# Kernel optimization log

Measured on AMD Instinct MI355X. Metric: run time of the kernel, lower is better.

## Reference

```python
import jax, jax.numpy as jnp
import numpy as np

EPS = 1e-12  # F.normalize eps

def _l2norm(t):
    n = jnp.linalg.norm(t, axis=-1, keepdims=True)
    return t / jnp.maximum(n, EPS)

def setup_inputs() -> dict:
    key = jax.random.key(0)
    ks = jax.random.split(key, 6)
    B, S, H, M = 4, 4096, 1024, 256
    x = jax.random.normal(ks[0], (B, S, H), dtype=jnp.float32)
    W_query = jax.random.normal(ks[1], (M, H), dtype=jnp.float32) * 0.02
    W_key = jax.random.normal(ks[2], (M, H), dtype=jnp.float32) * 0.02
    W_value = jax.random.normal(ks[3], (M, H), dtype=jnp.float32) * 0.02
    W_out = jax.random.normal(ks[4], (H, M), dtype=jnp.float32) * 0.02
    M0 = jnp.zeros((M, M), dtype=jnp.float32)
    return {"x": x, "W_query": W_query, "W_key": W_key, "W_value": W_value,
            "W_out": W_out, "M0": M0, "chunk_size": 64}

def reference(x, W_query, W_key, W_value, W_out, M0, chunk_size):
    B, S, H = x.shape
    Mdim = W_query.shape[0]
    decay, max_m_norm = 0.99, 10.0
    q = jnp.einsum('bsh,mh->bsm', x, W_query)
    k = _l2norm(jnp.einsum('bsh,mh->bsm', x, W_key))
    v = _l2norm(jnp.einsum('bsh,mh->bsm', x, W_value))
    n_chunks = S // chunk_size
    c = chunk_size
    # (n_chunks, B, c, Mdim) so scan iterates over chunks
    qc = q.reshape(B, n_chunks, c, Mdim).transpose(1, 0, 2, 3)
    kc = k.reshape(B, n_chunks, c, Mdim).transpose(1, 0, 2, 3)
    vc = v.reshape(B, n_chunks, c, Mdim).transpose(1, 0, 2, 3)

    def step(Mst, qkv):
        qch, kch, vch = qkv
        # read with state at start of chunk: q @ M.T
        r = jnp.einsum('bcm,nm->bcn', qch, Mst)
        # uniform write, token-level aggregation
        outer = jnp.einsum('bci,bcj->ij', vch, kch) / (B * c)
        Mn = decay * Mst + outer
        nrm = jnp.linalg.norm(Mn)
        Mn = Mn * (max_m_norm / jnp.maximum(nrm, max_m_norm))
        return Mn, r

    _, r_all = jax.lax.scan(step, M0, (qc, kc, vc))  # (n_chunks, B, c, Mdim)
    retrieved = r_all.transpose(1, 0, 2, 3).reshape(B, S, Mdim)
    out = jnp.einsum('bsm,hm->bsh', retrieved, W_out)
    return out
```

## Files before the change

### kernel.cpp

```cpp
#include <hip/hip_runtime.h>
#include <hip/hip_bf16.h>


typedef __attribute__((ext_vector_type(4))) float  f4;
typedef __attribute__((ext_vector_type(8))) short  bf16x8;

constexpr int   Hdim  = 1024;
constexpr int   Md    = 256;
constexpr int   Ttok  = 16384;
constexpr float DECAY = 0.99f;
constexpr float MAXN  = 10.0f;

__device__ __forceinline__ unsigned short f2bf(float f) {
  union { float f; unsigned u; } v; v.f = f;
  unsigned r = v.u + 0x7FFFu + ((v.u >> 16) & 1u);
  return (unsigned short)(r >> 16);
}
__device__ __forceinline__ float bf2f(unsigned short h) {
  union { unsigned u; float f; } v; v.u = ((unsigned)h) << 16; return v.f;
}
__device__ __forceinline__ unsigned pk2bf(float a, float b) {
  __hip_bfloat162 h = __float22bfloat162_rn(make_float2(a, b));
  unsigned u; __builtin_memcpy(&u, &h, 4); return u;
}
__device__ __forceinline__ void gll16(const void* gptr, void* lptr) {
  __builtin_amdgcn_global_load_lds(
      (const __attribute__((address_space(1))) unsigned int*)gptr,
      (__attribute__((address_space(3))) unsigned int*)lptr, 16, 0, 0);
}

__global__ __launch_bounds__(256) void k0_wcvt(
    const float* __restrict__ Wq, const float* __restrict__ Wk,
    const float* __restrict__ Wv, const float* __restrict__ Wo,
    unsigned short* __restrict__ Wb, unsigned short* __restrict__ Wob)
{
  int gid = blockIdx.x * 256 + threadIdx.x;
  const float* src; unsigned short* dst; int off;
  if (gid < 32768)      { src = Wq; dst = Wb;          off = gid; }
  else if (gid < 65536) { src = Wk; dst = Wb + 262144; off = gid - 32768; }
  else if (gid < 98304) { src = Wv; dst = Wb + 524288; off = gid - 65536; }
  else                  { src = Wo; dst = Wob;         off = gid - 98304; }
  float4 a = ((const float4*)src)[off * 2];
  float4 b = ((const float4*)src)[off * 2 + 1];
  ((uint4*)dst)[off] = make_uint4(pk2bf(a.x, a.y), pk2bf(a.z, a.w),
                                  pk2bf(b.x, b.y), pk2bf(b.z, b.w));
}

__global__ __launch_bounds__(256) void k1_proj(
    const float* __restrict__ x, const unsigned short* __restrict__ Wb,
    unsigned short* __restrict__ qp, unsigned short* __restrict__ kb,
    unsigned short* __restrict__ vb)
{
  __shared__ float          As[128 * 64];
  __shared__ unsigned short Bs[128 * 64];
  const int tid = threadIdx.x;
  const int g = blockIdx.x;
  const int xcd = g & 7, wq_ = g >> 3;
  const int ntile = wq_ % 6;
  const int strip = xcd * 16 + wq_ / 6;
  const int row0 = strip * 128;
  const int n0 = ntile * 128;
  const int seg = n0 >> 8;
  const int nw0 = n0 & 255;
  unsigned short* dst = (seg == 0) ? qp : ((seg == 1) ? kb : vb);

  const int lane = tid & 63, wid = tid >> 6;
  const int wm = wid & 1, wn = wid >> 1;
  const int lr = lane & 15, lq = lane >> 4;
  const int arow_l = lane >> 4, aseg_l = lane & 15;
  const int brow_l = lane >> 3, bseg_l = lane & 7;

  f4 acc[4][4];
#pragma unroll
  for (int i = 0; i < 4; ++i)
#pragma unroll
    for (int j = 0; j < 4; ++j) acc[i][j] = f4{0.f, 0.f, 0.f, 0.f};

  for (int kk = 0; kk < Hdim; kk += 64) {
#pragma unroll
    for (int i = 0; i < 8; ++i) {
      int r = wid * 32 + i * 4 + arow_l;
      int s = aseg_l ^ (r & 15);
      gll16(&x[(long)(row0 + r) * Hdim + kk + s * 4], &As[(wid * 32 + i * 4) * 64]);
    }
#pragma unroll
    for (int i = 0; i < 4; ++i) {
      int r = wid * 32 + i * 8 + brow_l;
      int s = bseg_l ^ (r & 7);
      gll16(&Wb[(long)(n0 + r) * Hdim + kk + s * 8], &Bs[(wid * 32 + i * 8) * 64]);
    }
    __syncthreads();
#pragma unroll
    for (int ks = 0; ks < 2; ++ks) {
      bf16x8 af[4], bfr[4];
#pragma unroll
      for (int i = 0; i < 4; ++i) {
        int m = wm * 64 + i * 16 + lr;
        int p0 = (ks * 8 + lq * 2) ^ (m & 15);
        int p1 = p0 ^ 1;
        f4 a0 = *(const f4*)&As[m * 64 + p0 * 4];
        f4 a1 = *(const f4*)&As[m * 64 + p1 * 4];
        union { bf16x8 v; unsigned u[4]; } au;
        au.u[0] = pk2bf(a0[0], a0[1]); au.u[1] = pk2bf(a0[2], a0[3]);
        au.u[2] = pk2bf(a1[0], a1[1]); au.u[3] = pk2bf(a1[2], a1[3]);
        af[i] = au.v;
      }
#pragma unroll
      for (int j = 0; j < 4; ++j) {
        int n = wn * 64 + j * 16 + lr;
        int pb = (ks * 4 + lq) ^ (n & 7);
        bfr[j] = *(const bf16x8*)&Bs[n * 64 + pb * 8];
      }
#pragma unroll
      for (int i = 0; i < 4; ++i)
#pragma unroll
        for (int j = 0; j < 4; ++j)
          acc[i][j] = __builtin_amdgcn_mfma_f32_16x16x32_bf16(af[i], bfr[j], acc[i][j], 0, 0, 0);
    }
    __syncthreads();
  }
#pragma unroll
  for (int i = 0; i < 4; ++i)
#pragma unroll
    for (int rr = 0; rr < 4; ++rr) {
      int token = row0 + wm * 64 + i * 16 + lq * 4 + rr;
      int b = token >> 12, s = token & 4095;
      int pidx = (s >> 6) * 256 + b * 64 + (s & 63);
#pragma unroll
      for (int j = 0; j < 4; ++j) {
        int nn = nw0 + wn * 64 + j * 16 + lr;
        dst[(long)pidx * Md + nn] = f2bf(acc[i][j][rr]);
      }
    }
}

__global__ __launch_bounds__(256) void k2_norms(
    const unsigned short* __restrict__ kb, const unsigned short* __restrict__ vb,
    float* __restrict__ innk, float* __restrict__ innv, float* __restrict__ D)
{
  const int tid = threadIdx.x;
  if (blockIdx.x == 0)
    for (int i = tid; i < 4096; i += 256) D[i] = 0.f;
  const int wid = tid >> 6, lane = tid & 63;
  const int row = blockIdx.x * 4 + wid;
  const unsigned short* p = (row < Ttok) ? (kb + (long)row * Md) : (vb + (long)(row - Ttok) * Md);
  ushort4 v = *(const ushort4*)&p[lane * 4];
  float f0 = bf2f(v.x), f1 = bf2f(v.y), f2 = bf2f(v.z), f3 = bf2f(v.w);
  float s = f0 * f0 + f1 * f1 + f2 * f2 + f3 * f3;
#pragma unroll
  for (int off = 32; off; off >>= 1) s += __shfl_xor(s, off);
  if (lane == 0) {
    float inv = 1.0f / fmaxf(sqrtf(s), 1e-12f);
    if (row < Ttok) innk[row] = inv; else innv[row - Ttok] = inv;
  }
}

__global__ __launch_bounds__(256) void k3_outer(
    const unsigned short* __restrict__ kb, const unsigned short* __restrict__ vb,
    const float* __restrict__ innk, const float* __restrict__ innv,
    float* __restrict__ O)
{
  __shared__ unsigned short Als[64][40];
  __shared__ unsigned short Bls[256][40];
  const int tid = threadIdx.x;
  const int t  = blockIdx.y;
  const int i0 = blockIdx.x * 64;
  const int lane = tid & 63, wid = tid >> 6;
  const int lr = lane & 15, lq = lane >> 4;

  f4 acc[16];
#pragma unroll
  for (int q = 0; q < 16; ++q) acc[q] = f4{0.f, 0.f, 0.f, 0.f};

  for (int tok0 = 0; tok0 < 256; tok0 += 32) {
    {
      int i4 = (tid & 15) * 4, tl0 = tid >> 4;
#pragma unroll
      for (int p = 0; p < 2; ++p) {
        int tl = tl0 + 16 * p;
        int pidx = t * 256 + tok0 + tl;
        float sc = innv[pidx];
        ushort4 vv = *(const ushort4*)&vb[(long)pidx * Md + i0 + i4];
        Als[i4 + 0][tl] = f2bf(bf2f(vv.x) * sc);
        Als[i4 + 1][tl] = f2bf(bf2f(vv.y) * sc);
        Als[i4 + 2][tl] = f2bf(bf2f(vv.z) * sc);
        Als[i4 + 3][tl] = f2bf(bf2f(vv.w) * sc);
      }
    }
    {
      int j4 = (tid & 63) * 4, tl0 = tid >> 6;
#pragma unroll
      for (int p = 0; p < 8; ++p) {
        int tl = tl0 + 4 * p;
        int pidx = t * 256 + tok0 + tl;
        float sc = innk[pidx];
        ushort4 kv = *(const ushort4*)&kb[(long)pidx * Md + j4];
        Bls[j4 + 0][tl] = f2bf(bf2f(kv.x) * sc);
        Bls[j4 + 1][tl] = f2bf(bf2f(kv.y) * sc);
        Bls[j4 + 2][tl] = f2bf(bf2f(kv.z) * sc);
        Bls[j4 + 3][tl] = f2bf(bf2f(kv.w) * sc);
      }
    }
    __syncthreads();
    bf16x8 af = *(const bf16x8*)&Als[wid * 16 + lr][lq * 8];
#pragma unroll
    for (int j = 0; j < 16; ++j) {
      bf16x8 bfr = *(const bf16x8*)&Bls[j * 16 + lr][lq * 8];
      acc[j] = __builtin_amdgcn_mfma_f32_16x16x32_bf16(af, bfr, acc[j], 0, 0, 0);
    }
    __syncthreads();
  }
  float* Ot = O + (long)t * 65536;
#pragma unroll
  for (int j = 0; j < 16; ++j)
#pragma unroll
    for (int rr = 0; rr < 4; ++rr) {
      int i = i0 + wid * 16 + lq * 4 + rr;
      Ot[i * 256 + j * 16 + lr] = acc[j][rr] * (1.0f / 256.0f);
    }
}

__global__ __launch_bounds__(256) void k4_gram(const float* __restrict__ O, float* __restrict__ D)
{
  __shared__ unsigned short Tls[64][40];
  const int tid = threadIdx.x;
  const int kbase = blockIdx.x * 256;
  const int lane = tid & 63, wid = tid >> 6;
  const int lr = lane & 15, lq = lane >> 4;
  f4 acc[4];
#pragma unroll
  for (int q = 0; q < 4; ++q) acc[q] = f4{0.f, 0.f, 0.f, 0.f};

  for (int kk = 0; kk < 256; kk += 32) {
    int tk = tid & 7, tr = tid >> 3;
#pragma unroll
    for (int p = 0; p < 2; ++p) {
      int row = tr + 32 * p;
      float4 v = *(const float4*)&O[(long)row * 65536 + kbase + kk + tk * 4];
      *(uint2*)&Tls[row][tk * 4] = make_uint2(pk2bf(v.x, v.y), pk2bf(v.z, v.w));
    }
    __syncthreads();
    bf16x8 af = *(const bf16x8*)&Tls[wid * 16 + lr][lq * 8];
#pragma unroll
    for (int nt = 0; nt < 4; ++nt) {
      bf16x8 bfr = *(const bf16x8*)&Tls[nt * 16 + lr][lq * 8];
      acc[nt] = __builtin_amdgcn_mfma_f32_16x16x32_bf16(af, bfr, acc[nt], 0, 0, 0);
    }
    __syncthreads();
  }
#pragma unroll
  for (int nt = 0; nt < 4; ++nt)
#pragma unroll
    for (int rr = 0; rr < 4; ++rr)
      atomicAdd(&D[(wid * 16 + lq * 4 + rr) * 64 + nt * 16 + lr], acc[nt][rr]);
}

__global__ __launch_bounds__(256) void k56_mstate(const float* __restrict__ O,
    const float* __restrict__ D, unsigned short* __restrict__ Mb)
{
  __shared__ float Dl[64 * 65];
  __shared__ float sarr[64];
  const int tid = threadIdx.x;
  const int col = blockIdx.x * 256 + tid;
  float ov[64];
#pragma unroll
  for (int j = 0; j < 64; ++j) ov[j] = O[(long)j * 65536 + col];
  for (int i = tid; i < 4096; i += 256) Dl[(i >> 6) * 65 + (i & 63)] = D[i];
  __syncthreads();
  if (tid < 64) {
    const int lane = tid;
    float w = 0.f, nm2 = 0.f;
    for (int t = 0; t < 64; ++t) {
      float wt   = __shfl(w, t);
      float Dtt  = Dl[t * 65 + t];
      float nmn2 = DECAY * DECAY * nm2 + 2.f * DECAY * wt + Dtt;
      float nrm  = sqrtf(fmaxf(nmn2, 0.f));
      float s    = MAXN / fmaxf(nrm, MAXN);
      if (lane == 0) sarr[t] = s;
      w   = s * (DECAY * w + Dl[t * 65 + lane]);
      nm2 = s * s * nmn2;
    }
  }
  __syncthreads();
  float m = 0.f;
#pragma unroll
  for (int t = 0; t < 64; ++t) {
    Mb[(long)t * 65536 + col] = f2bf(m);
    m = sarr[t] * (DECAY * m + ov[t]);
  }
}

__global__ __launch_bounds__(256) void k7_rgemm(
    const unsigned short* __restrict__ qp, const unsigned short* __restrict__ Mb,
    unsigned short* __restrict__ rb)
{
  __shared__ unsigned short As[128 * 64];
  __shared__ unsigned short Bs[128 * 64];
  const int tid = threadIdx.x;
  const int t = blockIdx.z;
  const int row0 = t * 256 + blockIdx.y * 128;
  const int n0 = blockIdx.x * 128;
  const unsigned short* Bsrc = Mb + (long)t * 65536;
  const int lane = tid & 63, wid = tid >> 6;
  const int wm = wid & 1, wn = wid >> 1;
  const int lr = lane & 15, lq = lane >> 4;
  const int brow_l = lane >> 3, bseg_l = lane & 7;

  f4 acc[4][4];
#pragma unroll
  for (int i = 0; i < 4; ++i)
#pragma unroll
    for (int j = 0; j < 4; ++j) acc[i][j] = f4{0.f, 0.f, 0.f, 0.f};

  for (int kk = 0; kk < Md; kk += 64) {
#pragma unroll
    for (int i = 0; i < 4; ++i) {
      int r = wid * 32 + i * 8 + brow_l;
      int s = bseg_l ^ (r & 7);
      gll16(&qp[(long)(row0 + r) * Md + kk + s * 8], &As[(wid * 32 + i * 8) * 64]);
      gll16(&Bsrc[(long)(n0 + r) * Md + kk + s * 8], &Bs[(wid * 32 + i * 8) * 64]);
    }
    __syncthreads();
#pragma unroll
    for (int ks = 0; ks < 2; ++ks) {
      bf16x8 af[4], bfr[4];
#pragma unroll
      for (int i = 0; i < 4; ++i) {
        int m = wm * 64 + i * 16 + lr;
        int pa = (ks * 4 + lq) ^ (m & 7);
        af[i] = *(const bf16x8*)&As[m * 64 + pa * 8];
      }
#pragma unroll
      for (int j = 0; j < 4; ++j) {
        int n = wn * 64 + j * 16 + lr;
        int pb = (ks * 4 + lq) ^ (n & 7);
        bfr[j] = *(const bf16x8*)&Bs[n * 64 + pb * 8];
      }
#pragma unroll
      for (int i = 0; i < 4; ++i)
#pragma unroll
        for (int j = 0; j < 4; ++j)
          acc[i][j] = __builtin_amdgcn_mfma_f32_16x16x32_bf16(af[i], bfr[j], acc[i][j], 0, 0, 0);
    }
    __syncthreads();
  }
#pragma unroll
  for (int i = 0; i < 4; ++i)
#pragma unroll
    for (int rr = 0; rr < 4; ++rr) {
      int prow = row0 + wm * 64 + i * 16 + lq * 4 + rr;
#pragma unroll
      for (int j = 0; j < 4; ++j) {
        int n = n0 + wn * 64 + j * 16 + lr;
        rb[(long)prow * Md + n] = f2bf(acc[i][j][rr]);
      }
    }
}

__global__ __launch_bounds__(256) void k8_out(
    const unsigned short* __restrict__ rb, const unsigned short* __restrict__ Wob,
    float* __restrict__ out)
{
  __shared__ unsigned short As[128 * 64];
  __shared__ unsigned short Bs[128 * 64];
  const int tid = threadIdx.x;
  const int g = blockIdx.x;
  const int xcd = g & 7, wq_ = g >> 3;
  const int ntile = wq_ & 7;
  const int strip = xcd * 16 + (wq_ >> 3);
  const int n0 = ntile * 128;
  const int row0 = strip * 128;
  const int lane = tid & 63, wid = tid >> 6;
  const int wm = wid & 1, wn = wid >> 1;
  const int lr = lane & 15, lq = lane >> 4;
  const int brow_l = lane >> 3, bseg_l = lane & 7;

  f4 acc[4][4];
#pragma unroll
  for (int i = 0; i < 4; ++i)
#pragma unroll
    for (int j = 0; j < 4; ++j) acc[i][j] = f4{0.f, 0.f, 0.f, 0.f};

  for (int kk = 0; kk < Md; kk += 64) {
#pragma unroll
    for (int i = 0; i < 4; ++i) {
      int r = wid * 32 + i * 8 + brow_l;
      int s = bseg_l ^ (r & 7);
      gll16(&rb[(long)(row0 + r) * Md + kk + s * 8], &As[(wid * 32 + i * 8) * 64]);
      gll16(&Wob[(long)(n0 + r) * Md + kk + s * 8], &Bs[(wid * 32 + i * 8) * 64]);
    }
    __syncthreads();
#pragma unroll
    for (int ks = 0; ks < 2; ++ks) {
      bf16x8 af[4], bfr[4];
#pragma unroll
      for (int i = 0; i < 4; ++i) {
        int m = wm * 64 + i * 16 + lr;
        int pa = (ks * 4 + lq) ^ (m & 7);
        af[i] = *(const bf16x8*)&As[m * 64 + pa * 8];
      }
#pragma unroll
      for (int j = 0; j < 4; ++j) {
        int n = wn * 64 + j * 16 + lr;
        int pb = (ks * 4 + lq) ^ (n & 7);
        bfr[j] = *(const bf16x8*)&Bs[n * 64 + pb * 8];
      }
#pragma unroll
      for (int i = 0; i < 4; ++i)
#pragma unroll
        for (int j = 0; j < 4; ++j)
          acc[i][j] = __builtin_amdgcn_mfma_f32_16x16x32_bf16(af[i], bfr[j], acc[i][j], 0, 0, 0);
    }
    __syncthreads();
  }
#pragma unroll
  for (int i = 0; i < 4; ++i)
#pragma unroll
    for (int rr = 0; rr < 4; ++rr) {
      int pidx = row0 + wm * 64 + i * 16 + lq * 4 + rr;
      int t = pidx >> 8, rm = pidx & 255;
      int token = (rm >> 6) * 4096 + t * 64 + (rm & 63);
#pragma unroll
      for (int j = 0; j < 4; ++j) {
        int h = n0 + wn * 64 + j * 16 + lr;
        out[(long)token * Hdim + h] = acc[i][j][rr];
      }
    }
}

extern "C" void kernel_launch(void* const* d_in, const int* in_sizes, int n_in,
                              void* d_out, int out_size, void* d_ws, size_t ws_size,
                              hipStream_t stream) {
  (void)in_sizes; (void)n_in; (void)out_size; (void)ws_size;
  const float* x  = (const float*)d_in[0];
  const float* Wq = (const float*)d_in[1];
  const float* Wk = (const float*)d_in[2];
  const float* Wv = (const float*)d_in[3];
  const float* Wo = (const float*)d_in[4];
  float* out = (float*)d_out;
  char* ws = (char*)d_ws;

  unsigned short* qp  = (unsigned short*)(ws + 0);
  unsigned short* kb  = (unsigned short*)(ws + 8388608);
  unsigned short* vb  = (unsigned short*)(ws + 16777216);
  float* O    = (float*)(ws + 25165824);
  float* D    = (float*)(ws + 41943040);
  float* innk = (float*)(ws + 41959424);
  float* innv = (float*)(ws + 42024960);
  unsigned short* Wb  = (unsigned short*)(ws + 42090496);
  unsigned short* Wob = (unsigned short*)(ws + 43663360);
  unsigned short* Mb = vb;
  unsigned short* rb = kb;

  k0_wcvt  <<<512,            256, 0, stream>>>(Wq, Wk, Wv, Wo, Wb, Wob);
  k1_proj  <<<768,            256, 0, stream>>>(x, Wb, qp, kb, vb);
  k2_norms <<<8192,           256, 0, stream>>>(kb, vb, innk, innv, D);
  k3_outer <<<dim3(4, 64),    256, 0, stream>>>(kb, vb, innk, innv, O);
  k4_gram  <<<256,            256, 0, stream>>>(O, D);
  k56_mstate<<<256,           256, 0, stream>>>(O, D, Mb);
  k7_rgemm <<<dim3(2, 2, 64), 256, 0, stream>>>(qp, Mb, rb);
  k8_out   <<<1024,           256, 0, stream>>>(rb, Wob, out);
}
```

Before: 251.4 us.

## Fuse k/v norm computation into projection epilogue and store k/v transposed

The projection epilogue now accumulates per-token sums of squares for k and v with shuffles and atomics, which removes the separate norms kernel. It also writes k and v in a per-chunk transposed layout. The outer-product kernel then loads tiles straight into LDS with swizzled global_load_lds and applies the combined inverse-norm scale to the A fragment in registers. The Gram kernel grid is doubled with half the K range per block, and D is zeroed by a memset. The trade-off is scattered 2-byte transposed stores and atomics in the projection epilogue, and the norms now come from fp32 accumulators rather than bf16-rounded values.

```diff
diff --git a/kernel.cpp b/kernel.cpp
--- a/kernel.cpp
+++ b/kernel.cpp
@@ -7,7 +7,6 @@
 
 constexpr int   Hdim  = 1024;
 constexpr int   Md    = 256;
-constexpr int   Ttok  = 16384;
 constexpr float DECAY = 0.99f;
 constexpr float MAXN  = 10.0f;
 
@@ -32,9 +31,12 @@
 __global__ __launch_bounds__(256) void k0_wcvt(
     const float* __restrict__ Wq, const float* __restrict__ Wk,
     const float* __restrict__ Wv, const float* __restrict__ Wo,
-    unsigned short* __restrict__ Wb, unsigned short* __restrict__ Wob)
+    unsigned short* __restrict__ Wb, unsigned short* __restrict__ Wob,
+    float* __restrict__ ssk, float* __restrict__ ssv)
 {
   int gid = blockIdx.x * 256 + threadIdx.x;
+  if (gid < 16384) ssk[gid] = 0.f;
+  else if (gid < 32768) ssv[gid - 16384] = 0.f;
   const float* src; unsigned short* dst; int off;
   if (gid < 32768)      { src = Wq; dst = Wb;          off = gid; }
   else if (gid < 65536) { src = Wk; dst = Wb + 262144; off = gid - 32768; }
@@ -48,8 +50,8 @@
 
 __global__ __launch_bounds__(256) void k1_proj(
     const float* __restrict__ x, const unsigned short* __restrict__ Wb,
-    unsigned short* __restrict__ qp, unsigned short* __restrict__ kb,
-    unsigned short* __restrict__ vb)
+    unsigned short* __restrict__ qp, unsigned short* __restrict__ kT,
+    unsigned short* __restrict__ vT, float* __restrict__ ssk, float* __restrict__ ssv)
 {
   __shared__ float          As[128 * 64];
   __shared__ unsigned short Bs[128 * 64];
@@ -62,7 +64,6 @@
   const int n0 = ntile * 128;
   const int seg = n0 >> 8;
   const int nw0 = n0 & 255;
-  unsigned short* dst = (seg == 0) ? qp : ((seg == 1) ? kb : vb);
 
   const int lane = tid & 63, wid = tid >> 6;
   const int wm = wid & 1, wn = wid >> 1;
@@ -119,104 +120,118 @@
     }
     __syncthreads();
   }
-#pragma unroll
-  for (int i = 0; i < 4; ++i)
-#pragma unroll
-    for (int rr = 0; rr < 4; ++rr) {
-      int token = row0 + wm * 64 + i * 16 + lq * 4 + rr;
-      int b = token >> 12, s = token & 4095;
-      int pidx = (s >> 6) * 256 + b * 64 + (s & 63);
-#pragma unroll
-      for (int j = 0; j < 4; ++j) {
-        int nn = nw0 + wn * 64 + j * 16 + lr;
-        dst[(long)pidx * Md + nn] = f2bf(acc[i][j][rr]);
-      }
-    }
-}
-
-__global__ __launch_bounds__(256) void k2_norms(
-    const unsigned short* __restrict__ kb, const unsigned short* __restrict__ vb,
-    float* __restrict__ innk, float* __restrict__ innv, float* __restrict__ D)
-{
-  const int tid = threadIdx.x;
-  if (blockIdx.x == 0)
-    for (int i = tid; i < 4096; i += 256) D[i] = 0.f;
-  const int wid = tid >> 6, lane = tid & 63;
-  const int row = blockIdx.x * 4 + wid;
-  const unsigned short* p = (row < Ttok) ? (kb + (long)row * Md) : (vb + (long)(row - Ttok) * Md);
-  ushort4 v = *(const ushort4*)&p[lane * 4];
-  float f0 = bf2f(v.x), f1 = bf2f(v.y), f2 = bf2f(v.z), f3 = bf2f(v.w);
-  float s = f0 * f0 + f1 * f1 + f2 * f2 + f3 * f3;
-#pragma unroll
-  for (int off = 32; off; off >>= 1) s += __shfl_xor(s, off);
-  if (lane == 0) {
-    float inv = 1.0f / fmaxf(sqrtf(s), 1e-12f);
-    if (row < Ttok) innk[row] = inv; else innv[row - Ttok] = inv;
+
+  if (seg == 0) {
+#pragma unroll
+    for (int i = 0; i < 4; ++i)
+#pragma unroll
+      for (int rr = 0; rr < 4; ++rr) {
+        int token = row0 + wm * 64 + i * 16 + lq * 4 + rr;
+        int b = token >> 12, s = token & 4095;
+        int pidx = (s >> 6) * 256 + b * 64 + (s & 63);
+#pragma unroll
+        for (int j = 0; j < 4; ++j) {
+          int nn = nw0 + wn * 64 + j * 16 + lr;
+          qp[(long)pidx * Md + nn] = f2bf(acc[i][j][rr]);
+        }
+      }
+  } else {
+    unsigned short* dT = (seg == 1) ? kT : vT;
+    float* ss = (seg == 1) ? ssk : ssv;
+#pragma unroll
+    for (int i = 0; i < 4; ++i)
+#pragma unroll
+      for (int rr = 0; rr < 4; ++rr) {
+        int token = row0 + wm * 64 + i * 16 + lq * 4 + rr;
+        int b = token >> 12, s = token & 4095;
+        int pidx = (s >> 6) * 256 + b * 64 + (s & 63);
+        int tch = pidx >> 8, tin = pidx & 255;
+        float sq = 0.f;
+#pragma unroll
+        for (int j = 0; j < 4; ++j) {
+          int nn = nw0 + wn * 64 + j * 16 + lr;
+          float vv = acc[i][j][rr];
+          dT[(long)tch * 65536 + nn * 256 + tin] = f2bf(vv);
+          sq += vv * vv;
+        }
+        sq += __shfl_xor(sq, 1); sq += __shfl_xor(sq, 2);
+        sq += __shfl_xor(sq, 4); sq += __shfl_xor(sq, 8);
+        if (lr == 0) atomicAdd(&ss[pidx], sq);
+      }
   }
 }
 
 __global__ __launch_bounds__(256) void k3_outer(
-    const unsigned short* __restrict__ kb, const unsigned short* __restrict__ vb,
-    const float* __restrict__ innk, const float* __restrict__ innv,
+    const unsigned short* __restrict__ kT, const unsigned short* __restrict__ vT,
+    const float* __restrict__ ssk, const float* __restrict__ ssv,
     float* __restrict__ O)
 {
-  __shared__ unsigned short Als[64][40];
-  __shared__ unsigned short Bls[256][40];
-  const int tid = threadIdx.x;
-  const int t  = blockIdx.y;
+  __shared__ unsigned short As[64 * 64];
+  __shared__ unsigned short Bs[256 * 64];
+  __shared__ float sLs[256];
+  const int tid = threadIdx.x;
+  const int t = blockIdx.y;
   const int i0 = blockIdx.x * 64;
   const int lane = tid & 63, wid = tid >> 6;
   const int lr = lane & 15, lq = lane >> 4;
+  const int drow = lane >> 3, dseg = lane & 7;
+
+  {
+    float a = ssv[t * 256 + tid], b = ssk[t * 256 + tid];
+    sLs[tid] = rsqrtf(fmaxf(a, 1e-24f)) * rsqrtf(fmaxf(b, 1e-24f));
+  }
 
   f4 acc[16];
 #pragma unroll
   for (int q = 0; q < 16; ++q) acc[q] = f4{0.f, 0.f, 0.f, 0.f};
 
-  for (int tok0 = 0; tok0 < 256; tok0 += 32) {
-    {
-      int i4 = (tid & 15) * 4, tl0 = tid >> 4;
-#pragma unroll
-      for (int p = 0; p < 2; ++p) {
-        int tl = tl0 + 16 * p;
-        int pidx = t * 256 + tok0 + tl;
-        float sc = innv[pidx];
-        ushort4 vv = *(const ushort4*)&vb[(long)pidx * Md + i0 + i4];
-        Als[i4 + 0][tl] = f2bf(bf2f(vv.x) * sc);
-        Als[i4 + 1][tl] = f2bf(bf2f(vv.y) * sc);
-        Als[i4 + 2][tl] = f2bf(bf2f(vv.z) * sc);
-        Als[i4 + 3][tl] = f2bf(bf2f(vv.w) * sc);
-      }
-    }
-    {
-      int j4 = (tid & 63) * 4, tl0 = tid >> 6;
-#pragma unroll
-      for (int p = 0; p < 8; ++p) {
-        int tl = tl0 + 4 * p;
-        int pidx = t * 256 + tok0 + tl;
-        float sc = innk[pidx];
-        ushort4 kv = *(const ushort4*)&kb[(long)pidx * Md + j4];
-        Bls[j4 + 0][tl] = f2bf(bf2f(kv.x) * sc);
-        Bls[j4 + 1][tl] = f2bf(bf2f(kv.y) * sc);
-        Bls[j4 + 2][tl] = f2bf(bf2f(kv.z) * sc);
-        Bls[j4 + 3][tl] = f2bf(bf2f(kv.w) * sc);
-      }
-    }
-    __syncthreads();
-    bf16x8 af = *(const bf16x8*)&Als[wid * 16 + lr][lq * 8];
-#pragma unroll
-    for (int j = 0; j < 16; ++j) {
-      bf16x8 bfr = *(const bf16x8*)&Bls[j * 16 + lr][lq * 8];
-      acc[j] = __builtin_amdgcn_mfma_f32_16x16x32_bf16(af, bfr, acc[j], 0, 0, 0);
+  for (int tok0 = 0; tok0 < 256; tok0 += 64) {
+#pragma unroll
+    for (int j = 0; j < 2; ++j) {
+      int r = wid * 16 + j * 8 + drow;
+      int s = dseg ^ (r & 7);
+      gll16(&vT[(long)t * 65536 + (i0 + r) * 256 + tok0 + s * 8],
+            &As[(wid * 16 + j * 8) * 64]);
+    }
+#pragma unroll
+    for (int j = 0; j < 8; ++j) {
+      int r = wid * 64 + j * 8 + drow;
+      int s = dseg ^ (r & 7);
+      gll16(&kT[(long)t * 65536 + r * 256 + tok0 + s * 8],
+            &Bs[(wid * 64 + j * 8) * 64]);
+    }
+    __syncthreads();
+#pragma unroll
+    for (int ks = 0; ks < 2; ++ks) {
+      int m = wid * 16 + lr;
+      int pa = (ks * 4 + lq) ^ (m & 7);
+      bf16x8 ar = *(const bf16x8*)&As[m * 64 + pa * 8];
+      f4 s0 = *(const f4*)&sLs[tok0 + ks * 32 + lq * 8];
+      f4 s1 = *(const f4*)&sLs[tok0 + ks * 32 + lq * 8 + 4];
+      union { bf16x8 v; unsigned short e[8]; unsigned u[4]; } au;
+      au.v = ar;
+      au.u[0] = pk2bf(bf2f(au.e[0]) * s0[0], bf2f(au.e[1]) * s0[1]);
+      au.u[1] = pk2bf(bf2f(au.e[2]) * s0[2], bf2f(au.e[3]) * s0[3]);
+      au.u[2] = pk2bf(bf2f(au.e[4]) * s1[0], bf2f(au.e[5]) * s1[1]);
+      au.u[3] = pk2bf(bf2f(au.e[6]) * s1[2], bf2f(au.e[7]) * s1[3]);
+      bf16x8 af = au.v;
+#pragma unroll
+      for (int jf = 0; jf < 16; ++jf) {
+        int n = jf * 16 + lr;
+        int pb = (ks * 4 + lq) ^ (n & 7);
+        bf16x8 bfr = *(const bf16x8*)&Bs[n * 64 + pb * 8];
+        acc[jf] = __builtin_amdgcn_mfma_f32_16x16x32_bf16(af, bfr, acc[jf], 0, 0, 0);
+      }
     }
     __syncthreads();
   }
   float* Ot = O + (long)t * 65536;
 #pragma unroll
-  for (int j = 0; j < 16; ++j)
+  for (int jf = 0; jf < 16; ++jf)
 #pragma unroll
     for (int rr = 0; rr < 4; ++rr) {
       int i = i0 + wid * 16 + lq * 4 + rr;
-      Ot[i * 256 + j * 16 + lr] = acc[j][rr] * (1.0f / 256.0f);
+      Ot[i * 256 + jf * 16 + lr] = acc[jf][rr] * (1.0f / 256.0f);
     }
 }
 
@@ -224,14 +239,14 @@
 {
   __shared__ unsigned short Tls[64][40];
   const int tid = threadIdx.x;
-  const int kbase = blockIdx.x * 256;
+  const int kbase = blockIdx.x * 128;
   const int lane = tid & 63, wid = tid >> 6;
   const int lr = lane & 15, lq = lane >> 4;
   f4 acc[4];
 #pragma unroll
   for (int q = 0; q < 4; ++q) acc[q] = f4{0.f, 0.f, 0.f, 0.f};
 
-  for (int kk = 0; kk < 256; kk += 32) {
+  for (int kk = 0; kk < 128; kk += 32) {
     int tk = tid & 7, tr = tid >> 3;
 #pragma unroll
     for (int p = 0; p < 2; ++p) {
@@ -441,22 +456,22 @@
   char* ws = (char*)d_ws;
 
   unsigned short* qp  = (unsigned short*)(ws + 0);
-  unsigned short* kb  = (unsigned short*)(ws + 8388608);
-  unsigned short* vb  = (unsigned short*)(ws + 16777216);
+  unsigned short* kT  = (unsigned short*)(ws + 8388608);
+  unsigned short* vT  = (unsigned short*)(ws + 16777216);
   float* O    = (float*)(ws + 25165824);
   float* D    = (float*)(ws + 41943040);
-  float* innk = (float*)(ws + 41959424);
-  float* innv = (float*)(ws + 42024960);
+  float* ssk  = (float*)(ws + 41959424);
+  float* ssv  = (float*)(ws + 42024960);
   unsigned short* Wb  = (unsigned short*)(ws + 42090496);
   unsigned short* Wob = (unsigned short*)(ws + 43663360);
-  unsigned short* Mb = vb;
-  unsigned short* rb = kb;
-
-  k0_wcvt  <<<512,            256, 0, stream>>>(Wq, Wk, Wv, Wo, Wb, Wob);
-  k1_proj  <<<768,            256, 0, stream>>>(x, Wb, qp, kb, vb);
-  k2_norms <<<8192,           256, 0, stream>>>(kb, vb, innk, innv, D);
-  k3_outer <<<dim3(4, 64),    256, 0, stream>>>(kb, vb, innk, innv, O);
-  k4_gram  <<<256,            256, 0, stream>>>(O, D);
+  unsigned short* Mb = vT;
+  unsigned short* rb = kT;
+
+  hipMemsetAsync(D, 0, 64 * 64 * sizeof(float), stream);
+  k0_wcvt  <<<512,            256, 0, stream>>>(Wq, Wk, Wv, Wo, Wb, Wob, ssk, ssv);
+  k1_proj  <<<768,            256, 0, stream>>>(x, Wb, qp, kT, vT, ssk, ssv);
+  k3_outer <<<dim3(4, 64),    256, 0, stream>>>(kT, vT, ssk, ssv, O);
+  k4_gram  <<<512,            256, 0, stream>>>(O, D);
   k56_mstate<<<256,           256, 0, stream>>>(O, D, Mb);
   k7_rgemm <<<dim3(2, 2, 64), 256, 0, stream>>>(qp, Mb, rb);
   k8_out   <<<1024,           256, 0, stream>>>(rb, Wob, out);
```

New measurement: 256.6 us. 2.1% more time.
